# Kernel optimization log

Hardware: AMD Instinct MI355X
Metric: run time of the kernel (lower is better)

The kernel has to match this reference:

```python
import jax, jax.numpy as jnp
import numpy as np
from jax import lax

B, N, C = 8, 1024, 768
H, D = 12, 64
K = 3  # conv kernel size


def dwconv_over_batch(x, w, b):
    """Faithful port of SpatialDepthWisePerHeadConvolution as used in this module.
    x: [B, N, H, D]. The original code treats dim0 (B) as the conv length axis.
    w: [H*D, 1, K] depthwise kernel, b: [H*D].
    Returns [B, N, H, D].
    """
    b_, n_, h_, d_ = x.shape
    xc = jnp.transpose(x, (1, 2, 3, 0)).reshape(n_, h_ * d_, b_)  # [N, HD, B]
    y = lax.conv_general_dilated(
        xc, w, window_strides=(1,), padding=[(K - 1, K - 1)],
        feature_group_count=h_ * d_, dimension_numbers=("NCH", "OIH", "NCH"))
    y = y[:, :, :b_] + b[None, :, None]  # causal slice (drop last K-1)
    return jnp.transpose(y.reshape(n_, h_, d_, b_), (3, 0, 1, 2))


def setup_inputs() -> dict:
    key = jax.random.key(0)
    ks = jax.random.split(key, 12)
    s = 0.02
    inp = {
        "x": jax.random.normal(ks[0], (B, N, C), jnp.float32),
        "wq": jax.random.normal(ks[1], (C, H * D), jnp.float32) * s,
        "wk": jax.random.normal(ks[2], (C, H * D), jnp.float32) * s,
        "wv": jax.random.normal(ks[3], (C, H * D), jnp.float32) * s,
        "bv": jnp.zeros((H * D,), jnp.float32),
        "cq_w": jax.random.normal(ks[4], (H * D, 1, K), jnp.float32) * s,
        "cq_b": jnp.zeros((H * D,), jnp.float32),
        "ck_w": jax.random.normal(ks[5], (H * D, 1, K), jnp.float32) * s,
        "ck_b": jnp.zeros((H * D,), jnp.float32),
        "cv_w": jax.random.normal(ks[6], (H * D, 1, K), jnp.float32) * s,
        "cv_b": jnp.zeros((H * D,), jnp.float32),
        "wo": jax.random.normal(ks[7], (C, C), jnp.float32) * s,
        "bo": jnp.zeros((C,), jnp.float32),
    }
    return inp


def reference(x, wq, wk, wv, bv, cq_w, cq_b, ck_w, ck_b, cv_w, cv_b, wo, bo):
    scale = (C // H) ** -0.5
    # linear -> [B,N,H,D]
    q = (x @ wq).reshape(B, N, H, D)
    k = (x @ wk).reshape(B, N, H, D)
    v = ((x @ wv) + bv).reshape(B, N, H, D)
    # per-head depthwise causal conv (over batch axis, as in the original code)
    q = dwconv_over_batch(q, cq_w, cq_b)
    k = dwconv_over_batch(k, ck_w, ck_b)
    v = dwconv_over_batch(v, cv_w, cv_b)
    # [B,H,N,D]
    q = jnp.transpose(q, (0, 2, 1, 3))
    k = jnp.transpose(k, (0, 2, 1, 3))
    v = jnp.transpose(v, (0, 2, 1, 3))
    scores = jnp.einsum("bhnd,bhmd->bhnm", q, k) * scale
    attn = jax.nn.softmax(scores, axis=-1)
    out = jnp.einsum("bhnm,bhmd->bhnd", attn, v)
    out = jnp.transpose(out, (0, 2, 1, 3)).reshape(B, N, C)
    return out @ wo + bo
```

## Files before the change

kernel.cpp:

```cpp
#include <hip/hip_runtime.h>
#include <math.h>

static constexpr int B_ = 8, N_ = 1024, C_ = 768, H_ = 12, D_ = 64;

typedef __bf16 bf16_t;
typedef bf16_t bf16x8 __attribute__((ext_vector_type(8)));
typedef bf16_t bf16x4 __attribute__((ext_vector_type(4)));
typedef short short4v __attribute__((ext_vector_type(4)));
typedef float f32x4 __attribute__((ext_vector_type(4)));

#define MFMA32(a, b, c) __builtin_amdgcn_mfma_f32_16x16x32_bf16((a), (b), (c), 0, 0, 0)
#define MFMA16(a, b, c) __builtin_amdgcn_mfma_f32_16x16x16bf16_1k( \
    __builtin_bit_cast(short4v, (a)), __builtin_bit_cast(short4v, (b)), (c), 0, 0, 0)

__device__ __forceinline__ unsigned short f2bf(float f) {
    unsigned u = __builtin_bit_cast(unsigned, f);
    u += 0x7FFFu + ((u >> 16) & 1u);
    return (unsigned short)(u >> 16);
}

__device__ __forceinline__ float bf2f(unsigned short u) {
    return __builtin_bit_cast(float, (unsigned)u << 16);
}

__device__ __forceinline__ void gload16(void* lds, const void* g) {
    __builtin_amdgcn_global_load_lds(
        (const __attribute__((address_space(1))) unsigned int*)g,
        (__attribute__((address_space(3))) unsigned int*)lds, 16, 0, 0);
}

__device__ __forceinline__ int swz(int row, int kslot) {
    return row * 128 + (((kslot ^ row) & 7) << 4);
}

__global__ __launch_bounds__(256)
void castx_kernel(const float* __restrict__ in, unsigned short* __restrict__ out)
{
    const int i = blockIdx.x * 256 + threadIdx.x;
    const float4 a = ((const float4*)in)[2 * i];
    const float4 b = ((const float4*)in)[2 * i + 1];
    uint4 o;
    o.x = f2bf(a.x) | ((unsigned)f2bf(a.y) << 16);
    o.y = f2bf(a.z) | ((unsigned)f2bf(a.w) << 16);
    o.z = f2bf(b.x) | ((unsigned)f2bf(b.y) << 16);
    o.w = f2bf(b.z) | ((unsigned)f2bf(b.w) << 16);
    ((uint4*)out)[i] = o;
}

__global__ __launch_bounds__(256)
void castwT4_kernel(const float* w0, const float* w1, const float* w2, const float* w3,
                    unsigned short* o0, unsigned short* o1,
                    unsigned short* o2, unsigned short* o3)
{
    const float* w; unsigned short* wT;
    switch (blockIdx.z) {
        case 0:  w = w0; wT = o0; break;
        case 1:  w = w1; wT = o1; break;
        case 2:  w = w2; wT = o2; break;
        default: w = w3; wT = o3; break;
    }
    __shared__ float T[64][65];
    const int t = threadIdx.x;
    const int k0 = blockIdx.x * 64, n0 = blockIdx.y * 64;
    const int r = t >> 2, c0 = (t & 3) * 16;
#pragma unroll
    for (int j4 = 0; j4 < 4; ++j4) {
        const float4 v = *(const float4*)(w + (size_t)(k0 + r) * 768 + n0 + c0 + j4 * 4);
        T[r][c0 + j4 * 4 + 0] = v.x; T[r][c0 + j4 * 4 + 1] = v.y;
        T[r][c0 + j4 * 4 + 2] = v.z; T[r][c0 + j4 * 4 + 3] = v.w;
    }
    __syncthreads();
    const int nn = t >> 2;
    unsigned short o[16];
#pragma unroll
    for (int j = 0; j < 16; ++j) o[j] = f2bf(T[c0 + j][nn]);
    uint4* dst = (uint4*)(wT + (size_t)(n0 + nn) * 768 + k0 + c0);
    dst[0] = *(uint4*)(o); dst[1] = *(uint4*)(o + 8);
}

template <typename OutT>
__device__ __forceinline__ void gemm_body(const unsigned short* __restrict__ A,
                                          const unsigned short* __restrict__ BT,
                                          const float* __restrict__ bias,
                                          OutT* __restrict__ Cmat,
                                          int Ncols, int Kdim, int row0, int col0)
{
    __shared__ char As[128 * 128];
    __shared__ char Bs[128 * 128];

    const int tid = threadIdx.x, lane = tid & 63, w = tid >> 6;
    const int wr = w >> 1, wc = w & 1;
    const int slot = lane & 7, rsub = lane >> 3;

    f32x4 acc[4][4] = {};

    for (int k0 = 0; k0 < Kdim; k0 += 64) {
#pragma unroll
        for (int c = 0; c < 4; ++c) {
            const int chunk = c * 4 + w;
            const int r = chunk * 8 + rsub;
            gload16(As + chunk * 1024, A + (size_t)(row0 + r) * Kdim + k0 + 8 * (slot ^ (r & 7)));
            gload16(Bs + chunk * 1024, BT + (size_t)(col0 + r) * Kdim + k0 + 8 * (slot ^ (r & 7)));
        }
        __syncthreads();

#pragma unroll
        for (int kk = 0; kk < 2; ++kk) {
            const int kslot = kk * 4 + (lane >> 4);
            bf16x8 af[4], bf[4];
#pragma unroll
            for (int mi = 0; mi < 4; ++mi)
                af[mi] = *(const bf16x8*)(As + swz(wr * 64 + mi * 16 + (lane & 15), kslot));
#pragma unroll
            for (int ni = 0; ni < 4; ++ni)
                bf[ni] = *(const bf16x8*)(Bs + swz(wc * 64 + ni * 16 + (lane & 15), kslot));
#pragma unroll
            for (int mi = 0; mi < 4; ++mi)
#pragma unroll
                for (int ni = 0; ni < 4; ++ni)
                    acc[mi][ni] = MFMA32(af[mi], bf[ni], acc[mi][ni]);
        }
        __syncthreads();
    }

#pragma unroll
    for (int mi = 0; mi < 4; ++mi) {
        const int row = row0 + wr * 64 + mi * 16 + ((lane >> 4) << 2);
#pragma unroll
        for (int ni = 0; ni < 4; ++ni) {
            const int col = col0 + wc * 64 + ni * 16 + (lane & 15);
            const float bv_ = bias ? bias[col] : 0.f;
#pragma unroll
            for (int r = 0; r < 4; ++r) {
                const float v = acc[mi][ni][r] + bv_;
                if constexpr (sizeof(OutT) == 2)
                    Cmat[(size_t)(row + r) * Ncols + col] = (OutT)f2bf(v);
                else
                    Cmat[(size_t)(row + r) * Ncols + col] = v;
            }
        }
    }
}

__global__ __launch_bounds__(256)
void gemm_qkv(const unsigned short* __restrict__ xb,
              const unsigned short* __restrict__ wqT, const unsigned short* __restrict__ wkT,
              const unsigned short* __restrict__ wvT, const float* __restrict__ bv,
              unsigned short* __restrict__ q_lin, unsigned short* __restrict__ k_lin,
              unsigned short* __restrict__ v_lin)
{
    const int by = blockIdx.y, sel = by / 6, colt = by % 6;
    const unsigned short* BT; unsigned short* dst; const float* bias = nullptr;
    if (sel == 0)      { BT = wqT; dst = q_lin; }
    else if (sel == 1) { BT = wkT; dst = k_lin; }
    else               { BT = wvT; dst = v_lin; bias = bv; }
    gemm_body<unsigned short>(xb, BT, bias, dst, C_, C_, blockIdx.x * 128, colt * 128);
}

__global__ __launch_bounds__(256)
void gemm_proj(const unsigned short* __restrict__ A, const unsigned short* __restrict__ BT,
               const float* __restrict__ bias, float* __restrict__ Cmat)
{
    gemm_body<float>(A, BT, bias, Cmat, C_, C_, blockIdx.x * 128, blockIdx.y * 128);
}

__global__ __launch_bounds__(256)
void dwconv_qk(const unsigned short* __restrict__ qlin, const unsigned short* __restrict__ klin,
               const float* __restrict__ cq_w, const float* __restrict__ cq_b,
               const float* __restrict__ ck_w, const float* __restrict__ ck_b,
               unsigned short* __restrict__ qc, unsigned short* __restrict__ kc)
{
    const unsigned short* lin; const float* w; const float* bias;
    unsigned short* out;
    if (blockIdx.y == 0) { lin = qlin; w = cq_w; bias = cq_b; out = qc; }
    else                 { lin = klin; w = ck_w; bias = ck_b; out = kc; }

    const int i = blockIdx.x * 256 + threadIdx.x;
    const int c8 = i % (C_ / 8);
    const int n  = (i / (C_ / 8)) % N_;
    const int b  = i / ((C_ / 8) * N_);
    const int c  = c8 * 8;

    const uint4 z4 = make_uint4(0, 0, 0, 0);
    const uint4 x0 = (b >= 2) ? *(const uint4*)(lin + ((size_t)(b - 2) * N_ + n) * C_ + c) : z4;
    const uint4 x1 = (b >= 1) ? *(const uint4*)(lin + ((size_t)(b - 1) * N_ + n) * C_ + c) : z4;
    const uint4 x2 = *(const uint4*)(lin + ((size_t)b * N_ + n) * C_ + c);
    const unsigned short* u0 = (const unsigned short*)&x0;
    const unsigned short* u1 = (const unsigned short*)&x1;
    const unsigned short* u2 = (const unsigned short*)&x2;

    unsigned short y[8];
#pragma unroll
    for (int j = 0; j < 8; ++j) {
        const float v = w[(c + j) * 3 + 0] * bf2f(u0[j]) +
                        w[(c + j) * 3 + 1] * bf2f(u1[j]) +
                        w[(c + j) * 3 + 2] * bf2f(u2[j]) + bias[c + j];
        y[j] = f2bf(v);
    }
    const int h = c8 >> 3, d0 = (c8 & 7) * 8;
    *(uint4*)(out + (((size_t)b * H_ + h) * N_ + n) * 64 + d0) = *(uint4*)y;
}

__global__ __launch_bounds__(256)
void conv_v_transpose(const unsigned short* __restrict__ vlin, const float* __restrict__ w,
                      const float* __restrict__ bias, unsigned short* __restrict__ vt)
{
    __shared__ unsigned short T[64][72];
    const int t = threadIdx.x;
    const int n0 = blockIdx.x * 64, bh = blockIdx.y;
    const int b = bh / H_, h = bh % H_;
    const int r = t >> 2, c0 = (t & 3) * 16;
    const int cbase = h * 64 + c0;

    float acc[16];
#pragma unroll
    for (int i = 0; i < 16; ++i) acc[i] = bias[cbase + i];
#pragma unroll
    for (int j = 0; j < 3; ++j) {
        const int bb = b - 2 + j;
        if (bb < 0) continue;
        const unsigned short* src = vlin + ((size_t)bb * N_ + n0 + r) * C_ + cbase;
        const uint4 va = *(const uint4*)src;
        const uint4 vb2 = *(const uint4*)(src + 8);
        const unsigned short* u = (const unsigned short*)&va;
        const unsigned short* u2 = (const unsigned short*)&vb2;
#pragma unroll
        for (int i = 0; i < 8; ++i)  acc[i]     += w[(cbase + i) * 3 + j] * bf2f(u[i]);
#pragma unroll
        for (int i = 0; i < 8; ++i)  acc[8 + i] += w[(cbase + 8 + i) * 3 + j] * bf2f(u2[i]);
    }
    unsigned short tmp[16];
#pragma unroll
    for (int i = 0; i < 16; ++i) tmp[i] = f2bf(acc[i]);
    *(uint4*)&T[r][c0] = *(uint4*)tmp;
    *(uint4*)&T[r][c0 + 8] = *(uint4*)(tmp + 8);
    __syncthreads();

    const int d = t >> 2;
    unsigned short o[16];
#pragma unroll
    for (int i = 0; i < 16; ++i) o[i] = T[c0 + i][d];
    uint4* dst = (uint4*)(vt + ((size_t)bh * 64 + d) * N_ + n0 + c0);
    dst[0] = *(uint4*)o; dst[1] = *(uint4*)(o + 8);
}

__global__ __launch_bounds__(256)
void attn_mfma(const unsigned short* __restrict__ Qg, const unsigned short* __restrict__ Kg,
               const unsigned short* __restrict__ Vtg, unsigned short* __restrict__ Og)
{
    __shared__ char Kb[2][8192];
    __shared__ char Vb[2][8192];

    const int tid = threadIdx.x, lane = tid & 63, w = tid >> 6;
    const int g = lane >> 4, q = lane & 15;
    const int slot = lane & 7, rsub = lane >> 3;

    const int id = blockIdx.x;
    const int bh = (id & 7) * 12 + ((id >> 3) % 12);
    const int q0 = (id / 96) * 64;
    const int b = bh / H_, h = bh % H_;

    const unsigned short* Qp = Qg + (size_t)bh * N_ * 64;
    const unsigned short* Kp = Kg + (size_t)bh * N_ * 64;
    const unsigned short* Vp = Vtg + (size_t)bh * 64 * N_;

    bf16x8 qf[2];
#pragma unroll
    for (int kk = 0; kk < 2; ++kk)
        qf[kk] = *(const bf16x8*)(Qp + (size_t)(q0 + w * 16 + q) * 64 + kk * 32 + g * 8);

#pragma unroll
    for (int c = 0; c < 2; ++c) {
        const int chunk = c * 4 + w, r = chunk * 8 + rsub;
        gload16(Kb[0] + chunk * 1024, Kp + (size_t)r * 64 + 8 * (slot ^ (r & 7)));
        gload16(Vb[0] + chunk * 1024, Vp + (size_t)r * N_ + 8 * (slot ^ (r & 7)));
    }
    __syncthreads();

    f32x4 o[4] = {};
    float mrun = 0.f, lrun = 0.f;
    const float cs = 0.18033688011112042f;

    int buf = 0;
    for (int kt = 0; kt < N_ / 64; ++kt) {
        if (kt < N_ / 64 - 1) {
            const int nb = buf ^ 1;
#pragma unroll
            for (int c = 0; c < 2; ++c) {
                const int chunk = c * 4 + w, r = chunk * 8 + rsub;
                gload16(Kb[nb] + chunk * 1024, Kp + (size_t)((kt + 1) * 64 + r) * 64 + 8 * (slot ^ (r & 7)));
                gload16(Vb[nb] + chunk * 1024, Vp + (size_t)r * N_ + (kt + 1) * 64 + 8 * (slot ^ (r & 7)));
            }
        }

        f32x4 s[4] = {};
#pragma unroll
        for (int kk = 0; kk < 2; ++kk) {
            const int kslot = kk * 4 + g;
            bf16x8 kf[4];
#pragma unroll
            for (int ni = 0; ni < 4; ++ni)
                kf[ni] = *(const bf16x8*)(Kb[buf] + swz(ni * 16 + q, kslot));
#pragma unroll
            for (int ni = 0; ni < 4; ++ni)
                s[ni] = MFMA32(kf[ni], qf[kk], s[ni]);
        }

        bf16x4 pf[4];
        {
            float t[4][4];
#pragma unroll
            for (int ni = 0; ni < 4; ++ni)
#pragma unroll
                for (int rg = 0; rg < 4; ++rg) t[ni][rg] = s[ni][rg] * cs;
            float m0 = t[0][0];
#pragma unroll
            for (int ni = 0; ni < 4; ++ni)
#pragma unroll
                for (int rg = 0; rg < 4; ++rg) m0 = fmaxf(m0, t[ni][rg]);
            m0 = fmaxf(m0, __shfl_xor(m0, 16));
            m0 = fmaxf(m0, __shfl_xor(m0, 32));
            if (__any(m0 > mrun + 8.f)) {
                const float mnew = fmaxf(mrun, m0);
                const float f = exp2f(mrun - mnew);
                lrun *= f;
#pragma unroll
                for (int nd = 0; nd < 4; ++nd) o[nd] *= f;
                mrun = mnew;
            }
            float sum = 0.f;
#pragma unroll
            for (int ni = 0; ni < 4; ++ni) {
                const float p0 = exp2f(t[ni][0] - mrun);
                const float p1 = exp2f(t[ni][1] - mrun);
                const float p2 = exp2f(t[ni][2] - mrun);
                const float p3 = exp2f(t[ni][3] - mrun);
                sum += (p0 + p1) + (p2 + p3);
                bf16x4 pk;
                pk[0] = (bf16_t)p0; pk[1] = (bf16_t)p1; pk[2] = (bf16_t)p2; pk[3] = (bf16_t)p3;
                pf[ni] = pk;
            }
            sum += __shfl_xor(sum, 16);
            sum += __shfl_xor(sum, 32);
            lrun += sum;
        }

#pragma unroll
        for (int ni = 0; ni < 4; ++ni) {
            bf16x4 vf[4];
#pragma unroll
            for (int nd = 0; nd < 4; ++nd) {
                const int d = nd * 16 + q;
                vf[nd] = *(const bf16x4*)(Vb[buf] + d * 128 +
                          ((((2 * ni + (g >> 1)) ^ (d & 7))) << 4) + 8 * (g & 1));
            }
#pragma unroll
            for (int nd = 0; nd < 4; ++nd)
                o[nd] = MFMA16(vf[nd], pf[ni], o[nd]);
        }

        __syncthreads();
        buf ^= 1;
    }

    {
        const float inv = 1.0f / lrun;
        const int qrow = q0 + w * 16 + q;
        unsigned short* orow = Og + ((size_t)b * N_ + qrow) * C_ + h * D_;
#pragma unroll
        for (int nd = 0; nd < 4; ++nd) {
            unsigned short pk[4];
#pragma unroll
            for (int rg = 0; rg < 4; ++rg) pk[rg] = f2bf(o[nd][rg] * inv);
            *(uint2*)(orow + nd * 16 + 4 * g) = *(uint2*)pk;
        }
    }
}

extern "C" void kernel_launch(void* const* d_in, const int* in_sizes, int n_in,
                              void* d_out, int out_size, void* d_ws, size_t ws_size,
                              hipStream_t stream)
{
    (void)in_sizes; (void)n_in; (void)out_size; (void)ws_size;
    const float* x    = (const float*)d_in[0];
    const float* wq   = (const float*)d_in[1];
    const float* wk   = (const float*)d_in[2];
    const float* wv   = (const float*)d_in[3];
    const float* bv   = (const float*)d_in[4];
    const float* cq_w = (const float*)d_in[5];
    const float* cq_b = (const float*)d_in[6];
    const float* ck_w = (const float*)d_in[7];
    const float* ck_b = (const float*)d_in[8];
    const float* cv_w = (const float*)d_in[9];
    const float* cv_b = (const float*)d_in[10];
    const float* wo   = (const float*)d_in[11];
    const float* bo   = (const float*)d_in[12];
    float* out = (float*)d_out;

    char* wsb = (char*)d_ws;
    const size_t T  = (size_t)B_ * N_ * C_;
    const size_t WB = (size_t)2 * 589824;
    unsigned short* xb  = (unsigned short*)wsb;
    unsigned short* wqT = (unsigned short*)(wsb + 2 * T);
    unsigned short* wkT = wqT + 589824;
    unsigned short* wvT = wkT + 589824;
    unsigned short* woT = wvT + 589824;
    char* p = wsb + 2 * T + 4 * WB;
    unsigned short* q_lin = (unsigned short*)p;          p += 2 * T;
    unsigned short* k_lin = (unsigned short*)p;          p += 2 * T;
    unsigned short* v_lin = (unsigned short*)p;          p += 2 * T;
    unsigned short* qc    = (unsigned short*)p;          p += 2 * T;
    unsigned short* kc    = (unsigned short*)p;          p += 2 * T;
    unsigned short* vt    = (unsigned short*)p;          p += 2 * T;
    unsigned short* attn_out = xb;

    const int M = B_ * N_;

    castx_kernel<<<dim3((int)(T / 8 / 256)), 256, 0, stream>>>(x, xb);
    castwT4_kernel<<<dim3(12, 12, 4), 256, 0, stream>>>(wq, wk, wv, wo, wqT, wkT, wvT, woT);

    gemm_qkv<<<dim3(M / 128, 18), 256, 0, stream>>>(xb, wqT, wkT, wvT, bv, q_lin, k_lin, v_lin);

    dwconv_qk<<<dim3((int)(T / 8 / 256), 2), 256, 0, stream>>>(
        q_lin, k_lin, cq_w, cq_b, ck_w, ck_b, qc, kc);
    conv_v_transpose<<<dim3(N_ / 64, B_ * H_), 256, 0, stream>>>(v_lin, cv_w, cv_b, vt);

    attn_mfma<<<dim3(1536), 256, 0, stream>>>(qc, kc, vt, attn_out);

    gemm_proj<<<dim3(M / 128, C_ / 128), 256, 0, stream>>>(attn_out, woT, bo, out);
}
```

Baseline: 275.7 us.

## Add MFMA priority hints, XCD-aware GEMM block remap, and leaner softmax

After: 263.4 us. 1.05x faster.

```diff
diff --git a/kernel.cpp b/kernel.cpp
--- a/kernel.cpp
+++ b/kernel.cpp
@@ -114,11 +114,13 @@
 #pragma unroll
             for (int ni = 0; ni < 4; ++ni)
                 bf[ni] = *(const bf16x8*)(Bs + swz(wc * 64 + ni * 16 + (lane & 15), kslot));
+            __builtin_amdgcn_s_setprio(1);
 #pragma unroll
             for (int mi = 0; mi < 4; ++mi)
 #pragma unroll
                 for (int ni = 0; ni < 4; ++ni)
                     acc[mi][ni] = MFMA32(af[mi], bf[ni], acc[mi][ni]);
+            __builtin_amdgcn_s_setprio(0);
         }
         __syncthreads();
     }
@@ -149,19 +151,27 @@
               unsigned short* __restrict__ q_lin, unsigned short* __restrict__ k_lin,
               unsigned short* __restrict__ v_lin)
 {
-    const int by = blockIdx.y, sel = by / 6, colt = by % 6;
+    const int id = blockIdx.x;
+    const int j = id >> 3;
+    const int bx = (id & 7) * 8 + j / 18;
+    const int by = j % 18;
+    const int sel = by / 6, colt = by % 6;
     const unsigned short* BT; unsigned short* dst; const float* bias = nullptr;
     if (sel == 0)      { BT = wqT; dst = q_lin; }
     else if (sel == 1) { BT = wkT; dst = k_lin; }
     else               { BT = wvT; dst = v_lin; bias = bv; }
-    gemm_body<unsigned short>(xb, BT, bias, dst, C_, C_, blockIdx.x * 128, colt * 128);
+    gemm_body<unsigned short>(xb, BT, bias, dst, C_, C_, bx * 128, colt * 128);
 }
 
 __global__ __launch_bounds__(256)
 void gemm_proj(const unsigned short* __restrict__ A, const unsigned short* __restrict__ BT,
                const float* __restrict__ bias, float* __restrict__ Cmat)
 {
-    gemm_body<float>(A, BT, bias, Cmat, C_, C_, blockIdx.x * 128, blockIdx.y * 128);
+    const int id = blockIdx.x;
+    const int j = id >> 3;
+    const int bx = (id & 7) * 8 + j / 6;
+    const int by = j % 6;
+    gemm_body<float>(A, BT, bias, Cmat, C_, C_, bx * 128, by * 128);
 }
 
 __global__ __launch_bounds__(256)
@@ -301,48 +311,41 @@
 #pragma unroll
             for (int ni = 0; ni < 4; ++ni)
                 kf[ni] = *(const bf16x8*)(Kb[buf] + swz(ni * 16 + q, kslot));
+            __builtin_amdgcn_s_setprio(1);
 #pragma unroll
             for (int ni = 0; ni < 4; ++ni)
                 s[ni] = MFMA32(kf[ni], qf[kk], s[ni]);
+            __builtin_amdgcn_s_setprio(0);
         }
 
         bf16x4 pf[4];
         {
-            float t[4][4];
+            float m0 = s[0][0];
 #pragma unroll
             for (int ni = 0; ni < 4; ++ni)
 #pragma unroll
-                for (int rg = 0; rg < 4; ++rg) t[ni][rg] = s[ni][rg] * cs;
-            float m0 = t[0][0];
-#pragma unroll
-            for (int ni = 0; ni < 4; ++ni)
-#pragma unroll
-                for (int rg = 0; rg < 4; ++rg) m0 = fmaxf(m0, t[ni][rg]);
+                for (int rg = 0; rg < 4; ++rg) m0 = fmaxf(m0, s[ni][rg]);
             m0 = fmaxf(m0, __shfl_xor(m0, 16));
             m0 = fmaxf(m0, __shfl_xor(m0, 32));
-            if (__any(m0 > mrun + 8.f)) {
-                const float mnew = fmaxf(mrun, m0);
+            if (__any(m0 * cs > mrun + 8.f)) {
+                const float mnew = m0 * cs;
                 const float f = exp2f(mrun - mnew);
                 lrun *= f;
 #pragma unroll
                 for (int nd = 0; nd < 4; ++nd) o[nd] *= f;
                 mrun = mnew;
             }
-            float sum = 0.f;
 #pragma unroll
             for (int ni = 0; ni < 4; ++ni) {
-                const float p0 = exp2f(t[ni][0] - mrun);
-                const float p1 = exp2f(t[ni][1] - mrun);
-                const float p2 = exp2f(t[ni][2] - mrun);
-                const float p3 = exp2f(t[ni][3] - mrun);
-                sum += (p0 + p1) + (p2 + p3);
+                const float p0 = exp2f(fmaf(s[ni][0], cs, -mrun));
+                const float p1 = exp2f(fmaf(s[ni][1], cs, -mrun));
+                const float p2 = exp2f(fmaf(s[ni][2], cs, -mrun));
+                const float p3 = exp2f(fmaf(s[ni][3], cs, -mrun));
+                lrun += (p0 + p1) + (p2 + p3);
                 bf16x4 pk;
                 pk[0] = (bf16_t)p0; pk[1] = (bf16_t)p1; pk[2] = (bf16_t)p2; pk[3] = (bf16_t)p3;
                 pf[ni] = pk;
             }
-            sum += __shfl_xor(sum, 16);
-            sum += __shfl_xor(sum, 32);
-            lrun += sum;
         }
 
 #pragma unroll
@@ -354,9 +357,11 @@
                 vf[nd] = *(const bf16x4*)(Vb[buf] + d * 128 +
                           ((((2 * ni + (g >> 1)) ^ (d & 7))) << 4) + 8 * (g & 1));
             }
+            __builtin_amdgcn_s_setprio(1);
 #pragma unroll
             for (int nd = 0; nd < 4; ++nd)
                 o[nd] = MFMA16(vf[nd], pf[ni], o[nd]);
+            __builtin_amdgcn_s_setprio(0);
         }
 
         __syncthreads();
@@ -364,6 +369,8 @@
     }
 
     {
+        lrun += __shfl_xor(lrun, 16);
+        lrun += __shfl_xor(lrun, 32);
         const float inv = 1.0f / lrun;
         const int qrow = q0 + w * 16 + q;
         unsigned short* orow = Og + ((size_t)b * N_ + qrow) * C_ + h * D_;
@@ -419,7 +426,7 @@
     castx_kernel<<<dim3((int)(T / 8 / 256)), 256, 0, stream>>>(x, xb);
     castwT4_kernel<<<dim3(12, 12, 4), 256, 0, stream>>>(wq, wk, wv, wo, wqT, wkT, wvT, woT);
 
-    gemm_qkv<<<dim3(M / 128, 18), 256, 0, stream>>>(xb, wqT, wkT, wvT, bv, q_lin, k_lin, v_lin);
+    gemm_qkv<<<dim3((M / 128) * 18), 256, 0, stream>>>(xb, wqT, wkT, wvT, bv, q_lin, k_lin, v_lin);
 
     dwconv_qk<<<dim3((int)(T / 8 / 256), 2), 256, 0, stream>>>(
         q_lin, k_lin, cq_w, cq_b, ck_w, ck_b, qc, kc);
@@ -427,5 +434,5 @@
 
     attn_mfma<<<dim3(1536), 256, 0, stream>>>(qc, kc, vt, attn_out);
 
-    gemm_proj<<<dim3(M / 128, C_ / 128), 256, 0, stream>>>(attn_out, woT, bo, out);
-}
+    gemm_proj<<<dim3((M / 128) * 6), 256, 0, stream>>>(attn_out, woT, bo, out);
+}
```
